# Kernel tuning notes

Hardware: AMD Instinct MI355X
Metric: run time of the kernel (lower is better)

## Reference

```python
import jax, jax.numpy as jnp
import numpy as np

NV = 40962      # icosphere level 6 vertices: 10*4^6 + 2
NF = 81920      # faces: 2*(NV-2)
BS, CIN, COUT, NCOEFF = 8, 32, 64, 4


def _make_sparse(rng, n_rows, n_cols, nnz_per_row, scale):
    rows = np.repeat(np.arange(n_rows, dtype=np.int32), nnz_per_row)
    cols = rng.integers(0, n_cols, size=n_rows * nnz_per_row).astype(np.int32)
    vals = (rng.standard_normal(n_rows * nnz_per_row) * scale).astype(np.float32)
    return jnp.asarray(rows), jnp.asarray(cols), jnp.asarray(vals)


def setup_inputs() -> dict:
    key = jax.random.key(0)
    k_in, k_ew, k_ns, k_co = jax.random.split(key, 4)
    rng = np.random.default_rng(0)

    # G: [3*NF, NV], 3 nnz per row (face gradient from 3 incident vertices)
    G_rows, G_cols, G_vals = _make_sparse(rng, 3 * NF, NV, 3, 0.5)
    # L: [NV, NV], ~7 nnz per row (icosphere Laplacian stencil)
    L_rows, L_cols, L_vals = _make_sparse(rng, NV, NV, 7, 0.3)
    # F2V: [NV, NF], ~6 nnz per row (face-to-vertex averaging)
    F_rows, F_cols, F_vals = _make_sparse(rng, NV, NF, 6, 1.0 / 6.0)

    stdv = 1.0 / np.sqrt(CIN * NCOEFF)
    return {
        "input": jax.random.normal(k_in, (BS, CIN, NV), dtype=jnp.float32),
        "G_rows": G_rows, "G_cols": G_cols, "G_vals": G_vals,
        "L_rows": L_rows, "L_cols": L_cols, "L_vals": L_vals,
        "F_rows": F_rows, "F_cols": F_cols, "F_vals": F_vals,
        "EW": jax.random.normal(k_ew, (NF, 3), dtype=jnp.float32),
        "NS": jax.random.normal(k_ns, (NF, 3), dtype=jnp.float32),
        "coeffs": jax.random.uniform(k_co, (CIN * NCOEFF, COUT), dtype=jnp.float32,
                                     minval=-stdv, maxval=stdv),
        "nv_prev": NV,
        "nf": NF,
    }


def _spmatmul(x, rows, cols, vals, m):
    # x: [bs, c, n]; sparse op S: [m, n] in COO -> out: [bs, c, m]
    gathered = x[:, :, cols] * vals  # [bs, c, nnz]
    return jnp.zeros(x.shape[:2] + (m,), x.dtype).at[:, :, rows].add(gathered)


def reference(input, G_rows, G_cols, G_vals, L_rows, L_cols, L_vals,
              F_rows, F_cols, F_vals, EW, NS, coeffs, nv_prev, nf):
    bs, in_ch, _ = input.shape
    # per-face gradient: [bs, c, 3*nf] -> [bs, c, nf, 3]
    grad_face = _spmatmul(input, G_rows, G_cols, G_vals, 3 * nf)
    grad_face = grad_face.reshape(bs, in_ch, 3, nf).transpose(0, 1, 3, 2)
    laplacian = _spmatmul(input, L_rows, L_cols, L_vals, nv_prev)
    identity = input[..., :nv_prev]
    grad_face_ew = jnp.sum(grad_face * EW, axis=-1)  # [bs, c, nf]
    grad_face_ns = jnp.sum(grad_face * NS, axis=-1)
    grad_vert_ew = _spmatmul(grad_face_ew, F_rows, F_cols, F_vals, nv_prev)
    grad_vert_ns = _spmatmul(grad_face_ns, F_rows, F_cols, F_vals, nv_prev)
    feat = jnp.stack([identity, laplacian, grad_vert_ew, grad_vert_ns], axis=-1)  # [bs,c,nv,4]
    # dense projection; row-major flatten of (c,4) matches torch reshape ordering
    w = coeffs.reshape(in_ch, 4, -1)  # [c, 4, out]
    out = jnp.einsum('bcvk,cko->bov', feat, w)  # [bs, out, nv]  (bias unused in original forward)
    return out
```

## Files before the change

### kernel.cpp

```cpp
#include <hip/hip_runtime.h>

#define NV 40962
#define NF 81920
#define BSZ 8
#define CIN 32
#define COUT 64
#define BC 256

typedef unsigned short u16;
typedef float    f32x4 __attribute__((ext_vector_type(4)));
typedef _Float16 f16x8 __attribute__((ext_vector_type(8)));
typedef unsigned short u16x4 __attribute__((ext_vector_type(4)));
typedef unsigned short u16x8 __attribute__((ext_vector_type(8)));

__device__ __forceinline__ float bf2f(u16 h) {
    return __uint_as_float(((unsigned int)h) << 16);
}
__device__ __forceinline__ u16 f2bf(float f) {
    unsigned int u = __float_as_uint(f);
    unsigned int r = (u + 0x7fffu + ((u >> 16) & 1u)) >> 16;
    return (u16)r;
}

__global__ __launch_bounds__(256) void k_transpose(const float* __restrict__ in,
                                                   u16* __restrict__ xt) {
    __shared__ float tile[32][33];
    int c0 = blockIdx.x * 32;
    int r0 = blockIdx.y * 32;
    int tx = threadIdx.x & 31;
    int ty = threadIdx.x >> 5;
    #pragma unroll
    for (int i = 0; i < 32; i += 8) {
        int cc = c0 + tx;
        float v = 0.f;
        if (cc < NV) v = in[(size_t)(r0 + ty + i) * NV + cc];
        tile[ty + i][tx] = v;
    }
    __syncthreads();
    int t = threadIdx.x;
    #pragma unroll
    for (int e = t; e < 512; e += 256) {
        int vl = e >> 4;
        int p  = e & 15;
        int v  = c0 + vl;
        if (v < NV) {
            ushort2 val;
            val.x = f2bf(tile[p * 2][vl]);
            val.y = f2bf(tile[p * 2 + 1][vl]);
            *(ushort2*)&xt[(size_t)v * BC + r0 + p * 2] = val;
        }
    }
}

__global__ __launch_bounds__(256) void k_faces(const u16* __restrict__ xt,
                                               const int* __restrict__ Gc,
                                               const float* __restrict__ Gv,
                                               const float* __restrict__ EW,
                                               const float* __restrict__ NS,
                                               u16* __restrict__ gfi) {
    int t  = threadIdx.x;
    int f  = blockIdx.x * 4 + (t >> 6);
    int p4 = t & 63;
    int bc0 = p4 * 4;

    int   gc[9]; float gv[9];
    #pragma unroll
    for (int i = 0; i < 9; ++i) {
        int d = i / 3, j = i - d * 3;
        int base = 3 * (d * NF + f) + j;
        gc[i] = Gc[base];
        gv[i] = Gv[base];
    }
    float ewd[3], nsd[3];
    #pragma unroll
    for (int d = 0; d < 3; ++d) { ewd[d] = EW[f * 3 + d]; nsd[d] = NS[f * 3 + d]; }

    u16x4 xr[9];
    #pragma unroll
    for (int i = 0; i < 9; ++i)
        xr[i] = *(const u16x4*)&xt[(size_t)gc[i] * BC + bc0];

    float aew[4] = {0.f, 0.f, 0.f, 0.f}, ans[4] = {0.f, 0.f, 0.f, 0.f};
    #pragma unroll
    for (int d = 0; d < 3; ++d) {
        float g[4] = {0.f, 0.f, 0.f, 0.f};
        #pragma unroll
        for (int j = 0; j < 3; ++j) {
            float val = gv[d * 3 + j];
            #pragma unroll
            for (int k = 0; k < 4; ++k) g[k] += val * bf2f(xr[d * 3 + j][k]);
        }
        #pragma unroll
        for (int k = 0; k < 4; ++k) {
            aew[k] += ewd[d] * g[k];
            ans[k] += nsd[d] * g[k];
        }
    }
    u16x8 o;
    o[0] = f2bf(aew[0]); o[1] = f2bf(aew[1]); o[2] = f2bf(ans[0]); o[3] = f2bf(ans[1]);
    o[4] = f2bf(aew[2]); o[5] = f2bf(aew[3]); o[6] = f2bf(ans[2]); o[7] = f2bf(ans[3]);
    *(u16x8*)&gfi[(size_t)f * 512 + p4 * 8] = o;
}

#define VT 8
#define FROW 136
#define FBP  (16 * FROW)

__global__ __launch_bounds__(256, 4) void k_vertices(const u16* __restrict__ xt,
                                                  const int* __restrict__ Lc,
                                                  const float* __restrict__ Lv,
                                                  const int* __restrict__ Fc,
                                                  const float* __restrict__ Fv,
                                                  const u16* __restrict__ gfi,
                                                  const float* __restrict__ coeffs,
                                                  float* __restrict__ out) {
    __shared__ _Float16 fh[4 * FBP];
    int t = threadIdx.x;

    const int nwg = (NV + VT - 1) / VT;
    const int q = nwg >> 3, r = nwg & 7;
    int orig = blockIdx.x;
    int xcd = orig & 7, lid = orig >> 3;
    int swz = (xcd < r ? xcd * (q + 1) : r * (q + 1) + (xcd - r) * q) + lid;
    int v0 = swz * VT;

    int p4 = t & 63;
    int vg = t >> 6;
    int b  = p4 >> 3;
    int c4 = p4 & 7;
    int bc0 = p4 * 4;
    int bp = b >> 1;
    int rbase = (b & 1) * 8;
    int bkey = (b & 3) << 4;

    for (int vi = 0; vi < 2; ++vi) {
        int vloc = vg * 2 + vi;
        int v = v0 + vloc;
        float id[4]  = {0.f,0.f,0.f,0.f}, lp[4] = {0.f,0.f,0.f,0.f};
        float ew[4]  = {0.f,0.f,0.f,0.f}, ns[4] = {0.f,0.f,0.f,0.f};
        if (v < NV) {
            int   lc[7]; float lwv[7];
            #pragma unroll
            for (int j = 0; j < 7; ++j) { lc[j] = Lc[7 * v + j]; lwv[j] = Lv[7 * v + j]; }
            int   fc[6]; float fwv[6];
            #pragma unroll
            for (int j = 0; j < 6; ++j) { fc[j] = Fc[6 * v + j]; fwv[j] = Fv[6 * v + j]; }
            u16x4 xv = *(const u16x4*)&xt[(size_t)v * BC + bc0];
            u16x4 lt[7];
            #pragma unroll
            for (int j = 0; j < 7; ++j)
                lt[j] = *(const u16x4*)&xt[(size_t)lc[j] * BC + bc0];
            u16x8 ft[6];
            #pragma unroll
            for (int j = 0; j < 6; ++j)
                ft[j] = *(const u16x8*)&gfi[(size_t)fc[j] * 512 + p4 * 8];
            #pragma unroll
            for (int k = 0; k < 4; ++k) id[k] = bf2f(xv[k]);
            #pragma unroll
            for (int j = 0; j < 7; ++j)
                #pragma unroll
                for (int k = 0; k < 4; ++k) lp[k] += lwv[j] * bf2f(lt[j][k]);
            #pragma unroll
            for (int j = 0; j < 6; ++j) {
                float val = fwv[j];
                ew[0] += val * bf2f(ft[j][0]);  ew[1] += val * bf2f(ft[j][1]);
                ns[0] += val * bf2f(ft[j][2]);  ns[1] += val * bf2f(ft[j][3]);
                ew[2] += val * bf2f(ft[j][4]);  ew[3] += val * bf2f(ft[j][5]);
                ns[2] += val * bf2f(ft[j][6]);  ns[3] += val * bf2f(ft[j][7]);
            }
        }
        int row = rbase + vloc;
        int rowsh = bp * FBP + row * FROW;
        f16x8 h0, h1;
        h0[0]=(_Float16)id[0]; h0[1]=(_Float16)lp[0]; h0[2]=(_Float16)ew[0]; h0[3]=(_Float16)ns[0];
        h0[4]=(_Float16)id[1]; h0[5]=(_Float16)lp[1]; h0[6]=(_Float16)ew[1]; h0[7]=(_Float16)ns[1];
        h1[0]=(_Float16)id[2]; h1[1]=(_Float16)lp[2]; h1[2]=(_Float16)ew[2]; h1[3]=(_Float16)ns[2];
        h1[4]=(_Float16)id[3]; h1[5]=(_Float16)lp[3]; h1[6]=(_Float16)ew[3]; h1[7]=(_Float16)ns[3];
        *(f16x8*)&fh[rowsh + (((c4 * 32)      ^ bkey) >> 1)] = h0;
        *(f16x8*)&fh[rowsh + (((c4 * 32 + 16) ^ bkey) >> 1)] = h1;
    }

    int w  = vg;
    int l  = t & 63;
    int lr = l & 15;
    int lq = l >> 4;
    f16x8 Bh[4], Bl[4];
    #pragma unroll
    for (int ks = 0; ks < 4; ++ks) {
        #pragma unroll
        for (int e = 0; e < 8; ++e) {
            int k = ks * 32 + lq * 8 + e;
            float c = coeffs[k * 64 + w * 16 + lr];
            _Float16 h = (_Float16)c;
            Bh[ks][e] = h;
            Bl[ks][e] = (_Float16)(c - (float)h);
        }
    }
    __syncthreads();

    #pragma unroll
    for (int bp2 = 0; bp2 < 4; ++bp2) {
        int akey = ((bp2 * 2 + (lr >> 3)) & 3) << 4;
        f32x4 acc = {0.f, 0.f, 0.f, 0.f};
        #pragma unroll
        for (int ks = 0; ks < 4; ++ks) {
            int byteoff = (ks * 64 + lq * 16) ^ akey;
            f16x8 A = *(const f16x8*)&fh[bp2 * FBP + lr * FROW + (byteoff >> 1)];
            acc = __builtin_amdgcn_mfma_f32_16x16x32_f16(A, Bh[ks], acc, 0, 0, 0);
            acc = __builtin_amdgcn_mfma_f32_16x16x32_f16(A, Bl[ks], acc, 0, 0, 0);
        }
        int r0 = lq * 4;
        int bb = bp2 * 2 + (r0 >> 3);
        int vbase = v0 + (r0 & 7);
        int o = w * 16 + lr;
        size_t off = ((size_t)(bb * 64 + o)) * NV + vbase;
        if (v0 + VT <= NV) {
            *(float2*)&out[off]     = make_float2(acc.x, acc.y);
            *(float2*)&out[off + 2] = make_float2(acc.z, acc.w);
        } else {
            #pragma unroll
            for (int j = 0; j < 4; ++j)
                if (vbase + j < NV) out[off + j] = acc[j];
        }
    }
}

extern "C" void kernel_launch(void* const* d_in, const int* in_sizes, int n_in,
                              void* d_out, int out_size, void* d_ws, size_t ws_size,
                              hipStream_t stream) {
    (void)in_sizes; (void)n_in; (void)out_size; (void)ws_size;
    const float* input = (const float*)d_in[0];
    const int*   Gc = (const int*)d_in[2];
    const float* Gv = (const float*)d_in[3];
    const int*   Lc = (const int*)d_in[5];
    const float* Lv = (const float*)d_in[6];
    const int*   Fc = (const int*)d_in[8];
    const float* Fv = (const float*)d_in[9];
    const float* EW = (const float*)d_in[10];
    const float* NS = (const float*)d_in[11];
    const float* coeffs = (const float*)d_in[12];
    float* out = (float*)d_out;

    u16* ws  = (u16*)d_ws;
    u16* xt  = ws;
    u16* gfi = ws + (size_t)NV * BC;

    dim3 gA((NV + 31) / 32, BC / 32);
    k_transpose<<<gA, 256, 0, stream>>>(input, xt);

    k_faces<<<dim3(NF / 4), 256, 0, stream>>>(xt, Gc, Gv, EW, NS, gfi);

    k_vertices<<<dim3((NV + VT - 1) / VT), 256, 0, stream>>>(
        xt, Lc, Lv, Fc, Fv, gfi, coeffs, out);
}
```

Measured before the change: 151.0 us.

## Stage sparse indices in shared memory and batch gathers for two items per thread

Both the face and vertex kernels now load their sparse-matrix column indices and weights cooperatively into shared memory once per block, instead of having every lane redundantly load them. The face kernel processes 8 faces per block, 2 per wavefront, and all gathers for both items are issued before any arithmetic so more loads are in flight. The vertex kernel replaces the branchy per-vertex loop with branch-free masking and hoists all 2x(1+7+6) gathers ahead of the compute. The cost is higher register pressure from the larger live gather arrays, plus an extra barrier per block.

```diff
diff --git a/kernel.cpp b/kernel.cpp
--- a/kernel.cpp
+++ b/kernel.cpp
@@ -58,48 +58,65 @@
                                                const float* __restrict__ EW,
                                                const float* __restrict__ NS,
                                                u16* __restrict__ gfi) {
+    __shared__ int   sGc[3][24];
+    __shared__ float sGv[3][24];
+    __shared__ float sEW[24];
+    __shared__ float sNS[24];
     int t  = threadIdx.x;
-    int f  = blockIdx.x * 4 + (t >> 6);
-    int p4 = t & 63;
+    int f0 = blockIdx.x * 8;
+
+    if (t < 24) {
+        #pragma unroll
+        for (int d = 0; d < 3; ++d) {
+            sGc[d][t] = Gc[3 * (d * NF + f0) + t];
+            sGv[d][t] = Gv[3 * (d * NF + f0) + t];
+        }
+    } else if (t >= 32 && t < 56) {
+        sEW[t - 32] = EW[f0 * 3 + (t - 32)];
+        sNS[t - 32] = NS[f0 * 3 + (t - 32)];
+    }
+    __syncthreads();
+
+    int vg  = t >> 6;
+    int p4  = t & 63;
     int bc0 = p4 * 4;
 
-    int   gc[9]; float gv[9];
-    #pragma unroll
-    for (int i = 0; i < 9; ++i) {
-        int d = i / 3, j = i - d * 3;
-        int base = 3 * (d * NF + f) + j;
-        gc[i] = Gc[base];
-        gv[i] = Gv[base];
-    }
-    float ewd[3], nsd[3];
-    #pragma unroll
-    for (int d = 0; d < 3; ++d) { ewd[d] = EW[f * 3 + d]; nsd[d] = NS[f * 3 + d]; }
-
-    u16x4 xr[9];
-    #pragma unroll
-    for (int i = 0; i < 9; ++i)
-        xr[i] = *(const u16x4*)&xt[(size_t)gc[i] * BC + bc0];
-
-    float aew[4] = {0.f, 0.f, 0.f, 0.f}, ans[4] = {0.f, 0.f, 0.f, 0.f};
-    #pragma unroll
-    for (int d = 0; d < 3; ++d) {
-        float g[4] = {0.f, 0.f, 0.f, 0.f};
-        #pragma unroll
-        for (int j = 0; j < 3; ++j) {
-            float val = gv[d * 3 + j];
-            #pragma unroll
-            for (int k = 0; k < 4; ++k) g[k] += val * bf2f(xr[d * 3 + j][k]);
-        }
-        #pragma unroll
-        for (int k = 0; k < 4; ++k) {
-            aew[k] += ewd[d] * g[k];
-            ans[k] += nsd[d] * g[k];
-        }
-    }
-    u16x8 o;
-    o[0] = f2bf(aew[0]); o[1] = f2bf(aew[1]); o[2] = f2bf(ans[0]); o[3] = f2bf(ans[1]);
-    o[4] = f2bf(aew[2]); o[5] = f2bf(aew[3]); o[6] = f2bf(ans[2]); o[7] = f2bf(ans[3]);
-    *(u16x8*)&gfi[(size_t)f * 512 + p4 * 8] = o;
+    u16x4 xr[2][9];
+    #pragma unroll
+    for (int i = 0; i < 2; ++i) {
+        int fl = vg * 2 + i;
+        #pragma unroll
+        for (int e = 0; e < 9; ++e) {
+            int d = e / 3, j = e - d * 3;
+            int col = sGc[d][fl * 3 + j];
+            xr[i][e] = *(const u16x4*)&xt[(size_t)col * BC + bc0];
+        }
+    }
+    #pragma unroll
+    for (int i = 0; i < 2; ++i) {
+        int fl = vg * 2 + i;
+        float aew[4] = {0.f, 0.f, 0.f, 0.f}, ans[4] = {0.f, 0.f, 0.f, 0.f};
+        #pragma unroll
+        for (int d = 0; d < 3; ++d) {
+            float g[4] = {0.f, 0.f, 0.f, 0.f};
+            #pragma unroll
+            for (int j = 0; j < 3; ++j) {
+                float val = sGv[d][fl * 3 + j];
+                #pragma unroll
+                for (int k = 0; k < 4; ++k) g[k] += val * bf2f(xr[i][d * 3 + j][k]);
+            }
+            float ewd = sEW[fl * 3 + d], nsd = sNS[fl * 3 + d];
+            #pragma unroll
+            for (int k = 0; k < 4; ++k) {
+                aew[k] += ewd * g[k];
+                ans[k] += nsd * g[k];
+            }
+        }
+        u16x8 o;
+        o[0] = f2bf(aew[0]); o[1] = f2bf(aew[1]); o[2] = f2bf(ans[0]); o[3] = f2bf(ans[1]);
+        o[4] = f2bf(aew[2]); o[5] = f2bf(aew[3]); o[6] = f2bf(ans[2]); o[7] = f2bf(ans[3]);
+        *(u16x8*)&gfi[(size_t)(f0 + fl) * 512 + p4 * 8] = o;
+    }
 }
 
 #define VT 8
@@ -115,6 +132,10 @@
                                                   const float* __restrict__ coeffs,
                                                   float* __restrict__ out) {
     __shared__ _Float16 fh[4 * FBP];
+    __shared__ int   idxL[VT * 7];
+    __shared__ float wL[VT * 7];
+    __shared__ int   idxF[VT * 6];
+    __shared__ float wF[VT * 6];
     int t = threadIdx.x;
 
     const int nwg = (NV + VT - 1) / VT;
@@ -123,6 +144,19 @@
     int xcd = orig & 7, lid = orig >> 3;
     int swz = (xcd < r ? xcd * (q + 1) : r * (q + 1) + (xcd - r) * q) + lid;
     int v0 = swz * VT;
+
+    if (t < VT * 7) {
+        int gi = 7 * v0 + t;
+        bool ok = gi < 7 * NV;
+        idxL[t] = ok ? Lc[gi] : 0;
+        wL[t]   = ok ? Lv[gi] : 0.f;
+    } else if (t >= 64 && t < 64 + VT * 6) {
+        int gi = 6 * v0 + (t - 64);
+        bool ok = gi < 6 * NV;
+        idxF[t - 64] = ok ? Fc[gi] : 0;
+        wF[t - 64]   = ok ? Fv[gi] : 0.f;
+    }
+    __syncthreads();
 
     int p4 = t & 63;
     int vg = t >> 6;
@@ -133,44 +167,54 @@
     int rbase = (b & 1) * 8;
     int bkey = (b & 3) << 4;
 
-    for (int vi = 0; vi < 2; ++vi) {
-        int vloc = vg * 2 + vi;
+    int lc[2][7], fc[2][6];
+    #pragma unroll
+    for (int i = 0; i < 2; ++i) {
+        int vl = vg * 2 + i;
+        #pragma unroll
+        for (int j = 0; j < 7; ++j) lc[i][j] = idxL[vl * 7 + j];
+        #pragma unroll
+        for (int j = 0; j < 6; ++j) fc[i][j] = idxF[vl * 6 + j];
+    }
+    u16x4 xv[2];
+    u16x4 lt[2][7];
+    u16x8 ft[2][6];
+    #pragma unroll
+    for (int i = 0; i < 2; ++i) {
+        int v = v0 + vg * 2 + i;
+        int vs = v < NV ? v : 0;
+        xv[i] = *(const u16x4*)&xt[(size_t)vs * BC + bc0];
+        #pragma unroll
+        for (int j = 0; j < 7; ++j)
+            lt[i][j] = *(const u16x4*)&xt[(size_t)lc[i][j] * BC + bc0];
+        #pragma unroll
+        for (int j = 0; j < 6; ++j)
+            ft[i][j] = *(const u16x8*)&gfi[(size_t)fc[i][j] * 512 + p4 * 8];
+    }
+    #pragma unroll
+    for (int i = 0; i < 2; ++i) {
+        int vloc = vg * 2 + i;
         int v = v0 + vloc;
-        float id[4]  = {0.f,0.f,0.f,0.f}, lp[4] = {0.f,0.f,0.f,0.f};
-        float ew[4]  = {0.f,0.f,0.f,0.f}, ns[4] = {0.f,0.f,0.f,0.f};
-        if (v < NV) {
-            int   lc[7]; float lwv[7];
-            #pragma unroll
-            for (int j = 0; j < 7; ++j) { lc[j] = Lc[7 * v + j]; lwv[j] = Lv[7 * v + j]; }
-            int   fc[6]; float fwv[6];
-            #pragma unroll
-            for (int j = 0; j < 6; ++j) { fc[j] = Fc[6 * v + j]; fwv[j] = Fv[6 * v + j]; }
-            u16x4 xv = *(const u16x4*)&xt[(size_t)v * BC + bc0];
-            u16x4 lt[7];
-            #pragma unroll
-            for (int j = 0; j < 7; ++j)
-                lt[j] = *(const u16x4*)&xt[(size_t)lc[j] * BC + bc0];
-            u16x8 ft[6];
-            #pragma unroll
-            for (int j = 0; j < 6; ++j)
-                ft[j] = *(const u16x8*)&gfi[(size_t)fc[j] * 512 + p4 * 8];
-            #pragma unroll
-            for (int k = 0; k < 4; ++k) id[k] = bf2f(xv[k]);
-            #pragma unroll
-            for (int j = 0; j < 7; ++j)
-                #pragma unroll
-                for (int k = 0; k < 4; ++k) lp[k] += lwv[j] * bf2f(lt[j][k]);
-            #pragma unroll
-            for (int j = 0; j < 6; ++j) {
-                float val = fwv[j];
-                ew[0] += val * bf2f(ft[j][0]);  ew[1] += val * bf2f(ft[j][1]);
-                ns[0] += val * bf2f(ft[j][2]);  ns[1] += val * bf2f(ft[j][3]);
-                ew[2] += val * bf2f(ft[j][4]);  ew[3] += val * bf2f(ft[j][5]);
-                ns[2] += val * bf2f(ft[j][6]);  ns[3] += val * bf2f(ft[j][7]);
-            }
-        }
-        int row = rbase + vloc;
-        int rowsh = bp * FBP + row * FROW;
+        float valid = (v < NV) ? 1.f : 0.f;
+        float id[4], lp[4] = {0.f,0.f,0.f,0.f};
+        float ew[4] = {0.f,0.f,0.f,0.f}, ns[4] = {0.f,0.f,0.f,0.f};
+        #pragma unroll
+        for (int k = 0; k < 4; ++k) id[k] = valid * bf2f(xv[i][k]);
+        #pragma unroll
+        for (int j = 0; j < 7; ++j) {
+            float val = wL[vloc * 7 + j];
+            #pragma unroll
+            for (int k = 0; k < 4; ++k) lp[k] += val * bf2f(lt[i][j][k]);
+        }
+        #pragma unroll
+        for (int j = 0; j < 6; ++j) {
+            float val = wF[vloc * 6 + j];
+            ew[0] += val * bf2f(ft[i][j][0]);  ew[1] += val * bf2f(ft[i][j][1]);
+            ns[0] += val * bf2f(ft[i][j][2]);  ns[1] += val * bf2f(ft[i][j][3]);
+            ew[2] += val * bf2f(ft[i][j][4]);  ew[3] += val * bf2f(ft[i][j][5]);
+            ns[2] += val * bf2f(ft[i][j][6]);  ns[3] += val * bf2f(ft[i][j][7]);
+        }
+        int rowsh = bp * FBP + (rbase + vloc) * FROW;
         f16x8 h0, h1;
         h0[0]=(_Float16)id[0]; h0[1]=(_Float16)lp[0]; h0[2]=(_Float16)ew[0]; h0[3]=(_Float16)ns[0];
         h0[4]=(_Float16)id[1]; h0[5]=(_Float16)lp[1]; h0[6]=(_Float16)ew[1]; h0[7]=(_Float16)ns[1];
@@ -248,7 +292,7 @@
     dim3 gA((NV + 31) / 32, BC / 32);
     k_transpose<<<gA, 256, 0, stream>>>(input, xt);
 
-    k_faces<<<dim3(NF / 4), 256, 0, stream>>>(xt, Gc, Gv, EW, NS, gfi);
+    k_faces<<<dim3(NF / 8), 256, 0, stream>>>(xt, Gc, Gv, EW, NS, gfi);
 
     k_vertices<<<dim3((NV + VT - 1) / VT), 256, 0, stream>>>(
         xt, Lc, Lv, Fc, Fv, gfi, coeffs, out);
```

New measurement: 156.0 us. 1.03x slower.
